# Performance work log

Hardware: AMD Instinct MI355X
Metric: run time of the kernel (lower is better)

Reference implementation:

```python
import jax, jax.numpy as jnp
import numpy as np


def setup_inputs() -> dict:
    key = jax.random.key(0)
    ks = jax.random.split(key, 4)
    B, T, D, H, C = 256, 512, 128, 512, 128
    # xavier-uniform-like scales
    def xavier(k, shape):
        fan_in, fan_out = shape
        lim = np.sqrt(6.0 / (fan_in + fan_out))
        return jax.random.uniform(k, shape, jnp.float32, -lim, lim)
    return {
        "x": jax.random.normal(ks[0], (B, T, D), jnp.float32),
        "Whx": xavier(ks[1], (D, H)),
        "Whh": xavier(ks[2], (H, H)),
        "Wph": xavier(ks[3], (H, C)),
        "bh": jnp.zeros((H,), jnp.float32),
        "bp": jnp.zeros((C,), jnp.float32),
    }


def reference(x, Whx, Whh, Wph, bh, bp):
    B, T, D = x.shape
    H = Whh.shape[0]
    # Precompute input projections for all timesteps in one big GEMM: [B,T,H]
    xproj = jnp.einsum("btd,dh->bth", x, Whx) + bh

    def step(h, xp_t):
        h = jnp.tanh(xp_t + h @ Whh)
        return h, None

    h0 = jnp.zeros((B, H), x.dtype)
    # scan over time: xproj transposed to [T,B,H]
    h_final, _ = jax.lax.scan(step, h0, jnp.swapaxes(xproj, 0, 1))
    return h_final @ Wph + bp
```

## Files before the change

### kernel.cpp

```cpp
#include <hip/hip_runtime.h>
#include <type_traits>

typedef _Float16 f16;
typedef f16 f16x4 __attribute__((ext_vector_type(4)));
typedef f16 f16x8 __attribute__((ext_vector_type(8)));
typedef float f32x4 __attribute__((ext_vector_type(4)));
typedef unsigned int u32;

#define MFMA __builtin_amdgcn_mfma_f32_16x16x32_f16

constexpr int Bsz = 256, T = 512, D = 128, H = 512, C = 128;
constexpr int ROWS = 16;
constexpr int TPB  = 512;
constexpr int LDH  = H + 8;
constexpr int LDX  = D + 8;
constexpr int NTG  = H / 16;
constexpr int PKT  = 8;
constexpr int KTL  = 3;
constexpr size_t XSTRIDE = (size_t)16 * NTG * 256;

__global__ void pack_w(const float* __restrict__ W, int K, int N, f16* __restrict__ out) {
    int total = K * N;
    int NT = N / 16;
    for (int idx = blockIdx.x * blockDim.x + threadIdx.x; idx < total;
         idx += gridDim.x * blockDim.x) {
        int e    = idx & 7;
        int lane = (idx >> 3) & 63;
        int tile = idx >> 9;
        int kt = tile / NT, nt = tile % NT;
        int k = kt * 32 + 8 * (lane >> 4) + e;
        int n = nt * 16 + (lane & 15);
        out[idx] = (f16)W[(size_t)k * N + n];
    }
}

__device__ __forceinline__ f16x8 load_a(const f16* base, int ld, int kt, int l15, int l4) {
    return *(const f16x8*)(base + l15 * ld + kt * 32 + 8 * l4);
}

__device__ __forceinline__ float fast_tanh(float v) {
    float e = __expf(2.f * v);
    return 1.f - __fdividef(2.f, e + 1.f);
}

template <typename OT>
__global__ __launch_bounds__(TPB, 2) void xproj_k(
    const float* __restrict__ x, const f16* __restrict__ wpack,
    const float* __restrict__ bh, OT* __restrict__ xp) {
    const f16* Whx_p = wpack;
    __shared__ __align__(16) f16 xb[2][ROWS][LDX];
    const int tid = threadIdx.x, lane = tid & 63, w = tid >> 6;
    const int l15 = lane & 15, l4 = lane >> 4;
    const int bt = blockIdx.x;
    const int t0 = blockIdx.y * 16;
    const int b0 = bt * ROWS;
    const int xrow = tid >> 5, xd0 = (tid & 31) * 4;
    const int ntg0 = w * 4;

    float bh4[4];
#pragma unroll
    for (int nt = 0; nt < 4; nt++) bh4[nt] = bh[(ntg0 + nt) * 16 + l15];
    {
        float4 v = *(const float4*)&x[((size_t)(b0 + xrow) * T + t0) * D + xd0];
        f16x4 h4 = {(f16)v.x, (f16)v.y, (f16)v.z, (f16)v.w};
        *(f16x4*)&xb[0][xrow][xd0] = h4;
    }
    __syncthreads();

    int p = 0;
    for (int tt = 0; tt < 16; tt++) {
        int t = t0 + tt;
        float4 xv;
        const bool havex = (tt + 1 < 16);
        if (havex)
            xv = *(const float4*)&x[((size_t)(b0 + xrow) * T + (t + 1)) * D + xd0];
        f32x4 acc[4];
#pragma unroll
        for (int nt = 0; nt < 4; nt++)
            acc[nt] = (f32x4){bh4[nt], bh4[nt], bh4[nt], bh4[nt]};
#pragma unroll
        for (int kt = 0; kt < D / 32; kt++) {
            f16x8 a = load_a(&xb[p][0][0], LDX, kt, l15, l4);
            const f16* btp = Whx_p + (((size_t)kt * NTG + ntg0) * 64 + lane) * 8;
#pragma unroll
            for (int nt = 0; nt < 4; nt++) {
                f16x8 b = *(const f16x8*)(btp + (size_t)nt * 512);
                acc[nt] = MFMA(a, b, acc[nt], 0, 0, 0);
            }
        }
        if (havex) {
            f16x4 h4 = {(f16)xv.x, (f16)xv.y, (f16)xv.z, (f16)xv.w};
            *(f16x4*)&xb[p ^ 1][xrow][xd0] = h4;
        }
        OT* op = xp + (((size_t)t * 16 + bt) * NTG + ntg0) * 256 + (size_t)lane * 4;
#pragma unroll
        for (int nt = 0; nt < 4; nt++) {
            if constexpr (std::is_same_v<OT, float>) {
                *(f32x4*)(op + (size_t)nt * 256) = acc[nt];
            } else {
                f16x4 v = {(f16)acc[nt][0], (f16)acc[nt][1], (f16)acc[nt][2],
                           (f16)acc[nt][3]};
                *(f16x4*)(op + (size_t)nt * 256) = v;
            }
        }
        __syncthreads();
        p ^= 1;
    }
}

template <int XP>
__global__ __launch_bounds__(TPB, 2) void rnn_main(
    const float* __restrict__ x, const f16* __restrict__ wpack,
    const void* __restrict__ xproj, const float* __restrict__ bh,
    const float* __restrict__ bp, float* __restrict__ out) {
    const f16* Whx_p = wpack;
    const f16* Whh_p = wpack + D * H;
    const f16* Wph_p = wpack + D * H + H * H;

    __shared__ __align__(16) f16 hbuf[2][ROWS][LDH];
    __shared__ __align__(16) f16 whh_lds[KTL * NTG * 64 * 8];
    __shared__ __align__(16) f16 xbuf[(XP == 0) ? 2 : 1][(XP == 0) ? ROWS : 1]
                                     [(XP == 0) ? LDX : 8];

    const int tid = threadIdx.x, lane = tid & 63, w = tid >> 6;
    const int l15 = lane & 15, l4 = lane >> 4;
    const int b0 = blockIdx.x * ROWS;
    const int xrow = tid >> 5, xd0 = (tid & 31) * 4;
    const int ntg0 = w * 4;

    f16x8 wreg[PKT][4];
#pragma unroll
    for (int kt = 0; kt < PKT; kt++)
#pragma unroll
        for (int nt = 0; nt < 4; nt++)
            wreg[kt][nt] =
                *(const f16x8*)(Whh_p + (((size_t)kt * NTG + ntg0 + nt) * 64 + lane) * 8);

    {
        const f16* src = Whh_p + (size_t)PKT * NTG * 512;
        for (int i = tid; i < KTL * NTG * 64; i += TPB)
            *(f16x8*)&whh_lds[(size_t)i * 8] = *(const f16x8*)(src + (size_t)i * 8);
    }
    for (int i = tid; i < ROWS * LDH; i += TPB) (&hbuf[0][0][0])[i] = (f16)0.f;

    float bh4[4];
    const float* xpf = nullptr;
    const f16* xph = nullptr;
    if constexpr (XP == 1) {
        xpf = (const float*)xproj + (((size_t)blockIdx.x * NTG + ntg0) * 64 + lane) * 4;
    } else if constexpr (XP == 2) {
        xph = (const f16*)xproj + (((size_t)blockIdx.x * NTG + ntg0) * 64 + lane) * 4;
    } else {
#pragma unroll
        for (int nt = 0; nt < 4; nt++) bh4[nt] = bh[(ntg0 + nt) * 16 + l15];
        float4 v = *(const float4*)&x[((size_t)(b0 + xrow) * T + 0) * D + xd0];
        f16x4 h4 = {(f16)v.x, (f16)v.y, (f16)v.z, (f16)v.w};
        *(f16x4*)&xbuf[0][xrow][xd0] = h4;
    }

    f16x8 sA[4], sB[4];
    {
        const f16* wb0 = Whh_p + ((size_t)ntg0 * 64 + lane) * 8;
#pragma unroll
        for (int nt = 0; nt < 4; nt++)
            sA[nt] = *(const f16x8*)(wb0 + ((size_t)11 * NTG + nt) * 512);
#pragma unroll
        for (int nt = 0; nt < 4; nt++)
            sB[nt] = *(const f16x8*)(wb0 + ((size_t)12 * NTG + nt) * 512);
    }
    __syncthreads();

    auto body = [&](int t, int pp, f16x8(&bA)[4], f16x8(&bB)[4]) {
        uintptr_t whu = (uintptr_t)Whh_p;
        asm volatile("" : "+s"(whu));
        const f16* wbase = (const f16*)whu + ((size_t)ntg0 * 64 + lane) * 8;
        u32 zo = 0;
        asm volatile("" : "+v"(zo));
        const f16x8* wlds = (const f16x8*)whh_lds + zo;

        f32x4 xr32[4];
        f16x4 xr16[4];
        if constexpr (XP == 1) {
            const float* xq = xpf + (size_t)t * XSTRIDE;
#pragma unroll
            for (int nt = 0; nt < 4; nt++) xr32[nt] = *(const f32x4*)(xq + (size_t)nt * 256);
        } else if constexpr (XP == 2) {
            const f16* xq = xph + (size_t)t * XSTRIDE;
#pragma unroll
            for (int nt = 0; nt < 4; nt++) xr16[nt] = *(const f16x4*)(xq + (size_t)nt * 256);
        }

        f32x4 acc[4];
        if constexpr (XP == 0) {
#pragma unroll
            for (int nt = 0; nt < 4; nt++)
                acc[nt] = (f32x4){bh4[nt], bh4[nt], bh4[nt], bh4[nt]};
        } else {
#pragma unroll
            for (int nt = 0; nt < 4; nt++) acc[nt] = (f32x4){0.f, 0.f, 0.f, 0.f};
        }

        const f16* hb = &hbuf[pp][0][0];

        if constexpr (XP == 0) {
            float4 xv;
            const bool havex = (t + 1 < T);
            if (havex)
                xv = *(const float4*)&x[((size_t)(b0 + xrow) * T + (t + 1)) * D + xd0];
            uintptr_t wxu = (uintptr_t)Whx_p;
            asm volatile("" : "+s"(wxu));
            const f16* wxs = (const f16*)wxu;
#pragma unroll
            for (int kt = 0; kt < D / 32; kt++) {
                f16x8 a = load_a(&xbuf[pp][0][0], LDX, kt, l15, l4);
                const f16* bt = wxs + (((size_t)kt * NTG + ntg0) * 64 + lane) * 8;
#pragma unroll
                for (int nt = 0; nt < 4; nt++) {
                    f16x8 b = *(const f16x8*)(bt + (size_t)nt * 512);
                    acc[nt] = MFMA(a, b, acc[nt], 0, 0, 0);
                }
            }
            if (havex) {
                f16x4 h4 = {(f16)xv.x, (f16)xv.y, (f16)xv.z, (f16)xv.w};
                *(f16x4*)&xbuf[pp ^ 1][xrow][xd0] = h4;
            }
        }

        auto LS = [&](int kt, f16x8(&bf)[4]) {
#pragma unroll
            for (int nt = 0; nt < 4; nt++)
                bf[nt] = *(const f16x8*)(wbase + ((size_t)kt * NTG + nt) * 512);
        };
        auto PK = [&](int kt) {
            f16x8 a = load_a(hb, LDH, kt, l15, l4);
#pragma unroll
            for (int nt = 0; nt < 4; nt++)
                acc[nt] = MFMA(a, wreg[kt][nt], acc[nt], 0, 0, 0);
        };
        auto CL = [&](int ktl) {
            f16x8 a = load_a(hb, LDH, PKT + ktl, l15, l4);
#pragma unroll
            for (int nt = 0; nt < 4; nt++)
                acc[nt] = MFMA(a, wlds[((size_t)ktl * NTG + ntg0 + nt) * 64 + lane],
                               acc[nt], 0, 0, 0);
        };
        auto CS = [&](int kt, f16x8(&bf)[4]) {
            f16x8 a = load_a(hb, LDH, kt, l15, l4);
#pragma unroll
            for (int nt = 0; nt < 4; nt++) acc[nt] = MFMA(a, bf[nt], acc[nt], 0, 0, 0);
        };

        PK(0); CS(11, bA); LS(13, bA);
        PK(1); CS(12, bB); LS(14, bB);
        PK(2); CL(0);
        PK(3); CL(1);
        PK(4); CL(2);
        PK(5); CS(13, bA); LS(15, bA);
        PK(6); CS(14, bB); LS(11, bB);
        PK(7); CS(15, bA); LS(12, bA);

#pragma unroll
        for (int nt = 0; nt < 4; nt++)
#pragma unroll
            for (int r = 0; r < 4; r++) {
                float v = acc[nt][r];
                if constexpr (XP == 1) v += xr32[nt][r];
                else if constexpr (XP == 2) v += (float)xr16[nt][r];
                float th = fast_tanh(v);
                hbuf[pp ^ 1][l4 * 4 + r][(ntg0 + nt) * 16 + l15] = (f16)th;
            }
        __syncthreads();
    };

    for (int t = 0; t < T; t += 2) {
        body(t, 0, sA, sB);
        body(t + 1, 1, sB, sA);
    }

    {
        float bpv = bp[w * 16 + l15];
        f32x4 acc = {bpv, bpv, bpv, bpv};
#pragma unroll 4
        for (int kt = 0; kt < H / 32; kt++) {
            f16x8 a = load_a(&hbuf[0][0][0], LDH, kt, l15, l4);
            f16x8 b = *(const f16x8*)(Wph_p + (((size_t)kt * (C / 16) + w) * 64 + lane) * 8);
            acc = MFMA(a, b, acc, 0, 0, 0);
        }
#pragma unroll
        for (int r = 0; r < 4; r++)
            out[(size_t)(b0 + l4 * 4 + r) * C + w * 16 + l15] = acc[r];
    }
}

extern "C" void kernel_launch(void* const* d_in, const int* in_sizes, int n_in,
                              void* d_out, int out_size, void* d_ws, size_t ws_size,
                              hipStream_t stream) {
    const float* x   = (const float*)d_in[0];
    const float* Whx = (const float*)d_in[1];
    const float* Whh = (const float*)d_in[2];
    const float* Wph = (const float*)d_in[3];
    const float* bh  = (const float*)d_in[4];
    const float* bp  = (const float*)d_in[5];

    f16* wp = (f16*)d_ws;
    pack_w<<<dim3(128), 256, 0, stream>>>(Whx, D, H, wp);
    pack_w<<<dim3(512), 256, 0, stream>>>(Whh, H, H, wp + D * H);
    pack_w<<<dim3(128), 256, 0, stream>>>(Wph, H, C, wp + D * H + H * H);

    const size_t wbytes = (size_t)(D * H + H * H + H * C) * sizeof(f16);
    const size_t xpel   = (size_t)T * 16 * NTG * 256;

    if (ws_size >= wbytes + xpel * sizeof(float)) {
        float* xpb = (float*)((char*)d_ws + wbytes);
        xproj_k<float><<<dim3(16, T / 16), TPB, 0, stream>>>(x, wp, bh, xpb);
        rnn_main<1><<<dim3(Bsz / ROWS), TPB, 0, stream>>>(x, wp, xpb, bh, bp,
                                                          (float*)d_out);
    } else if (ws_size >= wbytes + xpel * sizeof(f16)) {
        f16* xpb = (f16*)((char*)d_ws + wbytes);
        xproj_k<f16><<<dim3(16, T / 16), TPB, 0, stream>>>(x, wp, bh, xpb);
        rnn_main<2><<<dim3(Bsz / ROWS), TPB, 0, stream>>>(x, wp, xpb, bh, bp,
                                                          (float*)d_out);
    } else {
        rnn_main<0><<<dim3(Bsz / ROWS), TPB, 0, stream>>>(x, wp, nullptr, bh, bp,
                                                          (float*)d_out);
    }
}
```

Before: 1.652 ms.

## Replace per-step block barrier with per-wave LDS flags and triple-buffered hidden state

In the precomputed-projection variants, the per-timestep __syncthreads is replaced by per-wave progress flags in LDS. Each wave publishes its step counter with a release store, and consumers spin with acquire loads only before reading the K-slices produced by other waves. The hidden-state buffer becomes triple-buffered so a fast wave can write step t+1 while slower waves still read step t-1. The MFMA order is rearranged so each wave's remote dependencies are consumed as late as possible, at the cost of spin-wait overhead and a more fragile memory-ordering scheme.

```diff
diff --git a/kernel.cpp b/kernel.cpp
--- a/kernel.cpp
+++ b/kernel.cpp
@@ -117,8 +117,9 @@
     const f16* Whh_p = wpack + D * H;
     const f16* Wph_p = wpack + D * H + H * H;
 
-    __shared__ __align__(16) f16 hbuf[2][ROWS][LDH];
+    __shared__ __align__(16) f16 hbuf[3][ROWS][LDH];
     __shared__ __align__(16) f16 whh_lds[KTL * NTG * 64 * 8];
+    __shared__ u32 pflag[8];
     __shared__ __align__(16) f16 xbuf[(XP == 0) ? 2 : 1][(XP == 0) ? ROWS : 1]
                                      [(XP == 0) ? LDX : 8];
 
@@ -142,6 +143,7 @@
             *(f16x8*)&whh_lds[(size_t)i * 8] = *(const f16x8*)(src + (size_t)i * 8);
     }
     for (int i = tid; i < ROWS * LDH; i += TPB) (&hbuf[0][0][0])[i] = (f16)0.f;
+    if (tid < 8) pflag[tid] = 0u;
 
     float bh4[4];
     const float* xpf = nullptr;
@@ -170,7 +172,17 @@
     }
     __syncthreads();
 
-    auto body = [&](int t, int pp, f16x8(&bA)[4], f16x8(&bB)[4]) {
+    auto spin = [&](int v, u32 tgt) {
+        if constexpr (XP != 0) {
+            if (v != w)
+                while (__hip_atomic_load(&pflag[v], __ATOMIC_ACQUIRE,
+                                         __HIP_MEMORY_SCOPE_WORKGROUP) < tgt) {
+                }
+        }
+    };
+
+    auto body = [&](u32 t, const f16* hb, f16* hw, f16x8(&bA)[4], f16x8(&bB)[4],
+                    int pp) {
         uintptr_t whu = (uintptr_t)Whh_p;
         asm volatile("" : "+s"(whu));
         const f16* wbase = (const f16*)whu + ((size_t)ntg0 * 64 + lane) * 8;
@@ -199,8 +211,6 @@
 #pragma unroll
             for (int nt = 0; nt < 4; nt++) acc[nt] = (f32x4){0.f, 0.f, 0.f, 0.f};
         }
-
-        const f16* hb = &hbuf[pp][0][0];
 
         if constexpr (XP == 0) {
             float4 xv;
@@ -250,14 +260,17 @@
             for (int nt = 0; nt < 4; nt++) acc[nt] = MFMA(a, bf[nt], acc[nt], 0, 0, 0);
         };
 
-        PK(0); CS(11, bA); LS(13, bA);
-        PK(1); CS(12, bB); LS(14, bB);
-        PK(2); CL(0);
-        PK(3); CL(1);
-        PK(4); CL(2);
-        PK(5); CS(13, bA); LS(15, bA);
-        PK(6); CS(14, bB); LS(11, bB);
-        PK(7); CS(15, bA); LS(12, bA);
+        spin(0, t); PK(0); PK(1);
+        spin(5, t); CS(11, bA); LS(13, bA);
+        spin(1, t); PK(2); PK(3);
+        spin(6, t); CS(12, bB); LS(14, bB);
+        spin(2, t); PK(4); PK(5);
+                    CS(13, bA); LS(15, bA);
+        spin(3, t); PK(6); PK(7);
+                    CS(14, bB); LS(11, bB);
+        spin(4, t); CL(0); CL(1);
+                    CS(15, bA); LS(12, bA);
+                    CL(2);
 
 #pragma unroll
         for (int nt = 0; nt < 4; nt++)
@@ -267,22 +280,37 @@
                 if constexpr (XP == 1) v += xr32[nt][r];
                 else if constexpr (XP == 2) v += (float)xr16[nt][r];
                 float th = fast_tanh(v);
-                hbuf[pp ^ 1][l4 * 4 + r][(ntg0 + nt) * 16 + l15] = (f16)th;
-            }
-        __syncthreads();
+                hw[(l4 * 4 + r) * LDH + (ntg0 + nt) * 16 + l15] = (f16)th;
+            }
+        if constexpr (XP != 0) {
+            if (lane == 0)
+                __hip_atomic_store(&pflag[w], t + 1, __ATOMIC_RELEASE,
+                                   __HIP_MEMORY_SCOPE_WORKGROUP);
+        } else {
+            __syncthreads();
+        }
     };
 
-    for (int t = 0; t < T; t += 2) {
-        body(t, 0, sA, sB);
-        body(t + 1, 1, sB, sA);
-    }
-
+    f16* r0 = &hbuf[0][0][0];
+    f16* r1 = &hbuf[1][0][0];
+    f16* r2 = &hbuf[2][0][0];
+    for (u32 t = 0; t < T; t += 2) {
+        body(t,     r0, r1, sA, sB, 0);
+        body(t + 1, r1, r2, sB, sA, 1);
+        f16* n0 = r2; f16* n1 = r0; f16* n2 = r1;
+        r0 = n0; r1 = n1; r2 = n2;
+    }
+
+    if constexpr (XP != 0) {
+#pragma unroll
+        for (int v = 0; v < 8; v++) spin(v, (u32)T);
+    }
     {
         float bpv = bp[w * 16 + l15];
         f32x4 acc = {bpv, bpv, bpv, bpv};
 #pragma unroll 4
         for (int kt = 0; kt < H / 32; kt++) {
-            f16x8 a = load_a(&hbuf[0][0][0], LDH, kt, l15, l4);
+            f16x8 a = load_a(r0, LDH, kt, l15, l4);
             f16x8 b = *(const f16x8*)(Wph_p + (((size_t)kt * (C / 16) + w) * 64 + lane) * 8);
             acc = MFMA(a, b, acc, 0, 0, 0);
         }
```

Result: faster. 1.408 ms (-14.8%).

## Replace per-step block barrier with per-wave LDS flag handshake and ring buffer

Applied to the files above, without the earlier changes.

Each step's __syncthreads is replaced, on the precomputed-projection paths, by per-wave producer and consumer flags in LDS. Waves spin on these flags only for the K-chunks of h they need, and h lives in a 5-slot ring so fast waves can run up to four steps ahead. The K-chunk order is rotated per wave so each wave starts on its own freshly written chunk, and the weights moved out of LDS into streamed global loads shift from one chunk to two. The aim is to remove lock-step barrier stalls between waves, at the cost of spin-polling overhead, extra LDS for the ring, and more global weight traffic per step.

```diff
diff --git a/kernel.cpp b/kernel.cpp
--- a/kernel.cpp
+++ b/kernel.cpp
@@ -1,5 +1,6 @@
 #include <hip/hip_runtime.h>
 #include <type_traits>
+#include <utility>
 
 typedef _Float16 f16;
 typedef f16 f16x4 __attribute__((ext_vector_type(4)));
@@ -8,6 +9,7 @@
 typedef unsigned int u32;
 
 #define MFMA __builtin_amdgcn_mfma_f32_16x16x32_f16
+#define WGSCOPE __HIP_MEMORY_SCOPE_WORKGROUP
 
 constexpr int Bsz = 256, T = 512, D = 128, H = 512, C = 128;
 constexpr int ROWS = 16;
@@ -16,8 +18,40 @@
 constexpr int LDX  = D + 8;
 constexpr int NTG  = H / 16;
 constexpr int PKT  = 8;
-constexpr int KTL  = 3;
+constexpr int KTL  = 2;
+constexpr int NSTR = 6;
+constexpr int RING = 5;
+constexpr int SLOT = ROWS * LDH;
 constexpr size_t XSTRIDE = (size_t)16 * NTG * 256;
+
+struct Sched {
+    int kt[16];
+    int spin[16];
+    int sidx[16];
+    int skt[NSTR];
+};
+constexpr Sched make_sched(int V) {
+    Sched s{};
+    const int BASE[16] = {0, 10, 1, 11, 2, 3, 12, 4, 13, 5, 6, 14, 7, 15, 8, 9};
+    bool seen[8] = {};
+    seen[V] = true;
+    int si = 0;
+    for (int j = 0; j < 16; j++) {
+        int kt = (BASE[j] + 2 * V) & 15;
+        s.kt[j] = kt;
+        int u = kt >> 1;
+        s.spin[j] = seen[u] ? -1 : u;
+        seen[u] = true;
+        if (kt >= PKT + KTL) {
+            s.sidx[j] = si;
+            s.skt[si] = kt;
+            si++;
+        } else {
+            s.sidx[j] = -1;
+        }
+    }
+    return s;
+}
 
 __global__ void pack_w(const float* __restrict__ W, int K, int N, f16* __restrict__ out) {
     int total = K * N;
@@ -117,8 +151,10 @@
     const f16* Whh_p = wpack + D * H;
     const f16* Wph_p = wpack + D * H + H * H;
 
-    __shared__ __align__(16) f16 hbuf[2][ROWS][LDH];
+    __shared__ __align__(16) f16 hbuf[RING][ROWS][LDH];
     __shared__ __align__(16) f16 whh_lds[KTL * NTG * 64 * 8];
+    __shared__ int pflag[8];
+    __shared__ int cflag[8];
     __shared__ __align__(16) f16 xbuf[(XP == 0) ? 2 : 1][(XP == 0) ? ROWS : 1]
                                      [(XP == 0) ? LDX : 8];
 
@@ -126,7 +162,6 @@
     const int l15 = lane & 15, l4 = lane >> 4;
     const int b0 = blockIdx.x * ROWS;
     const int xrow = tid >> 5, xd0 = (tid & 31) * 4;
-    const int ntg0 = w * 4;
 
     f16x8 wreg[PKT][4];
 #pragma unroll
@@ -134,155 +169,223 @@
 #pragma unroll
         for (int nt = 0; nt < 4; nt++)
             wreg[kt][nt] =
-                *(const f16x8*)(Whh_p + (((size_t)kt * NTG + ntg0 + nt) * 64 + lane) * 8);
+                *(const f16x8*)(Whh_p + (((size_t)kt * NTG + w * 4 + nt) * 64 + lane) * 8);
 
     {
         const f16* src = Whh_p + (size_t)PKT * NTG * 512;
         for (int i = tid; i < KTL * NTG * 64; i += TPB)
             *(f16x8*)&whh_lds[(size_t)i * 8] = *(const f16x8*)(src + (size_t)i * 8);
     }
-    for (int i = tid; i < ROWS * LDH; i += TPB) (&hbuf[0][0][0])[i] = (f16)0.f;
+    for (int i = tid; i < SLOT; i += TPB) (&hbuf[0][0][0])[i] = (f16)0.f;
+    if (tid < 8) { pflag[tid] = 0; cflag[tid] = -1000; }
 
     float bh4[4];
     const float* xpf = nullptr;
     const f16* xph = nullptr;
     if constexpr (XP == 1) {
-        xpf = (const float*)xproj + (((size_t)blockIdx.x * NTG + ntg0) * 64 + lane) * 4;
+        xpf = (const float*)xproj + (((size_t)blockIdx.x * NTG + w * 4) * 64 + lane) * 4;
     } else if constexpr (XP == 2) {
-        xph = (const f16*)xproj + (((size_t)blockIdx.x * NTG + ntg0) * 64 + lane) * 4;
+        xph = (const f16*)xproj + (((size_t)blockIdx.x * NTG + w * 4) * 64 + lane) * 4;
     } else {
 #pragma unroll
-        for (int nt = 0; nt < 4; nt++) bh4[nt] = bh[(ntg0 + nt) * 16 + l15];
+        for (int nt = 0; nt < 4; nt++) bh4[nt] = bh[(w * 4 + nt) * 16 + l15];
         float4 v = *(const float4*)&x[((size_t)(b0 + xrow) * T + 0) * D + xd0];
         f16x4 h4 = {(f16)v.x, (f16)v.y, (f16)v.z, (f16)v.w};
         *(f16x4*)&xbuf[0][xrow][xd0] = h4;
     }
-
-    f16x8 sA[4], sB[4];
+    __syncthreads();
+
+    f16* const hbase = &hbuf[0][0][0];
+
+    auto run = [&](auto vc) {
+        constexpr int V = decltype(vc)::value;
+        constexpr Sched S = make_sched(V);
+        constexpr int ntg0 = V * 4;
+
+        auto pollp = [&](int tgt) -> u32 {
+            int f = __hip_atomic_load(&pflag[lane & 7], __ATOMIC_ACQUIRE, WGSCOPE);
+            return (u32)__ballot(f >= tgt) & 0xffu;
+        };
+        auto pollc = [&](int tgt) -> u32 {
+            int f = __hip_atomic_load(&cflag[lane & 7], __ATOMIC_ACQUIRE, WGSCOPE);
+            return (u32)__ballot(f >= tgt) & 0xffu;
+        };
+
+        f16x8 sb0[4], sb1[4];
+        {
+            const f16* wb0 = Whh_p + ((size_t)ntg0 * 64 + lane) * 8;
+#pragma unroll
+            for (int nt = 0; nt < 4; nt++)
+                sb0[nt] = *(const f16x8*)(wb0 + ((size_t)S.skt[0] * NTG + nt) * 512);
+#pragma unroll
+            for (int nt = 0; nt < 4; nt++)
+                sb1[nt] = *(const f16x8*)(wb0 + ((size_t)S.skt[1] * NTG + nt) * 512);
+        }
+
+        int sR = 0, sW = 1;
+#pragma unroll 1
+        for (int t = 0; t < T; t++) {
+            const f16* hb = hbase + sR * SLOT;
+            f16* hw = hbase + sW * SLOT;
+
+            uintptr_t whu = (uintptr_t)Whh_p;
+            asm volatile("" : "+s"(whu));
+            const f16* wbase = (const f16*)whu + ((size_t)ntg0 * 64 + lane) * 8;
+            u32 zo = 0;
+            asm volatile("" : "+v"(zo));
+            const f16x8* wlds = (const f16x8*)whh_lds + zo;
+
+            f32x4 xr32[4];
+            f16x4 xr16[4];
+            if constexpr (XP == 1) {
+                const float* xq = xpf + (size_t)t * XSTRIDE;
+#pragma unroll
+                for (int nt = 0; nt < 4; nt++)
+                    xr32[nt] = *(const f32x4*)(xq + (size_t)nt * 256);
+            } else if constexpr (XP == 2) {
+                const f16* xq = xph + (size_t)t * XSTRIDE;
+#pragma unroll
+                for (int nt = 0; nt < 4; nt++)
+                    xr16[nt] = *(const f16x4*)(xq + (size_t)nt * 256);
+            }
+
+            f32x4 acc[4];
+            if constexpr (XP == 0) {
+#pragma unroll
+                for (int nt = 0; nt < 4; nt++)
+                    acc[nt] = (f32x4){bh4[nt], bh4[nt], bh4[nt], bh4[nt]};
+            } else {
+#pragma unroll
+                for (int nt = 0; nt < 4; nt++) acc[nt] = (f32x4){0.f, 0.f, 0.f, 0.f};
+            }
+
+            if constexpr (XP == 0) {
+                float4 xv;
+                const bool havex = (t + 1 < T);
+                if (havex)
+                    xv = *(const float4*)&x[((size_t)(b0 + xrow) * T + (t + 1)) * D + xd0];
+                uintptr_t wxu = (uintptr_t)Whx_p;
+                asm volatile("" : "+s"(wxu));
+                const f16* wxs = (const f16*)wxu;
+#pragma unroll
+                for (int kt = 0; kt < D / 32; kt++) {
+                    f16x8 a = load_a(&xbuf[t & 1][0][0], LDX, kt, l15, l4);
+                    const f16* bt = wxs + (((size_t)kt * NTG + ntg0) * 64 + lane) * 8;
+#pragma unroll
+                    for (int nt = 0; nt < 4; nt++) {
+                        f16x8 b = *(const f16x8*)(bt + (size_t)nt * 512);
+                        acc[nt] = MFMA(a, b, acc[nt], 0, 0, 0);
+                    }
+                }
+                if (havex) {
+                    f16x4 h4 = {(f16)xv.x, (f16)xv.y, (f16)xv.z, (f16)xv.w};
+                    *(f16x4*)&xbuf[(t & 1) ^ 1][xrow][xd0] = h4;
+                }
+            }
+
+            u32 kmask = 1u << V;
+
+            auto pos = [&](auto jc) {
+                constexpr int j = decltype(jc)::value;
+                if constexpr (XP != 0 && S.spin[j] >= 0) {
+                    constexpr int u = S.spin[j];
+                    while (!((kmask >> u) & 1u)) kmask = pollp(t);
+                }
+                constexpr int kt = S.kt[j];
+                f16x8 a = load_a(hb, LDH, kt, l15, l4);
+                if constexpr (kt < PKT) {
+#pragma unroll
+                    for (int nt = 0; nt < 4; nt++)
+                        acc[nt] = MFMA(a, wreg[kt][nt], acc[nt], 0, 0, 0);
+                } else if constexpr (kt < PKT + KTL) {
+#pragma unroll
+                    for (int nt = 0; nt < 4; nt++)
+                        acc[nt] = MFMA(
+                            a, wlds[((size_t)(kt - PKT) * NTG + ntg0 + nt) * 64 + lane],
+                            acc[nt], 0, 0, 0);
+                } else {
+                    constexpr int i = S.sidx[j];
+                    constexpr int nk = S.skt[(i + 2) % NSTR];
+                    if constexpr ((i & 1) == 0) {
+#pragma unroll
+                        for (int nt = 0; nt < 4; nt++)
+                            acc[nt] = MFMA(a, sb0[nt], acc[nt], 0, 0, 0);
+#pragma unroll
+                        for (int nt = 0; nt < 4; nt++)
+                            sb0[nt] = *(const f16x8*)(wbase + ((size_t)nk * NTG + nt) * 512);
+                    } else {
+#pragma unroll
+                        for (int nt = 0; nt < 4; nt++)
+                            acc[nt] = MFMA(a, sb1[nt], acc[nt], 0, 0, 0);
+#pragma unroll
+                        for (int nt = 0; nt < 4; nt++)
+                            sb1[nt] = *(const f16x8*)(wbase + ((size_t)nk * NTG + nt) * 512);
+                    }
+                }
+            };
+#define POS(J) pos(std::integral_constant<int, J>{})
+            POS(0);  POS(1);  POS(2);  POS(3);
+            POS(4);  POS(5);  POS(6);  POS(7);
+            POS(8);  POS(9);  POS(10); POS(11);
+            POS(12); POS(13); POS(14); POS(15);
+#undef POS
+
+            if constexpr (XP != 0) {
+                if (lane == 0)
+                    __hip_atomic_store(&cflag[V], t, __ATOMIC_RELEASE, WGSCOPE);
+                int tgt = t - (RING - 1);
+                while (pollc(tgt) != 0xffu) {
+                }
+            }
+
+#pragma unroll
+            for (int nt = 0; nt < 4; nt++)
+#pragma unroll
+                for (int r = 0; r < 4; r++) {
+                    float v = acc[nt][r];
+                    if constexpr (XP == 1) v += xr32[nt][r];
+                    else if constexpr (XP == 2) v += (float)xr16[nt][r];
+                    float th = fast_tanh(v);
+                    hw[(l4 * 4 + r) * LDH + (ntg0 + nt) * 16 + l15] = (f16)th;
+                }
+            if constexpr (XP != 0) {
+                if (lane == 0)
+                    __hip_atomic_store(&pflag[V], t + 1, __ATOMIC_RELEASE, WGSCOPE);
+            } else {
+                __syncthreads();
+            }
+
+            sR = (sR + 1 == RING) ? 0 : sR + 1;
+            sW = (sW + 1 == RING) ? 0 : sW + 1;
+        }
+    };
+
+    switch (w) {
+        case 0: run(std::integral_constant<int, 0>{}); break;
+        case 1: run(std::integral_constant<int, 1>{}); break;
+        case 2: run(std::integral_constant<int, 2>{}); break;
+        case 3: run(std::integral_constant<int, 3>{}); break;
+        case 4: run(std::integral_constant<int, 4>{}); break;
+        case 5: run(std::integral_constant<int, 5>{}); break;
+        case 6: run(std::integral_constant<int, 6>{}); break;
+        default: run(std::integral_constant<int, 7>{}); break;
+    }
+
+    if constexpr (XP != 0) {
+        for (;;) {
+            int f = __hip_atomic_load(&pflag[lane & 7], __ATOMIC_ACQUIRE, WGSCOPE);
+            if (((u32)__ballot(f >= T) & 0xffu) == 0xffu) break;
+        }
+    } else {
+        __syncthreads();
+    }
     {
-        const f16* wb0 = Whh_p + ((size_t)ntg0 * 64 + lane) * 8;
-#pragma unroll
-        for (int nt = 0; nt < 4; nt++)
-            sA[nt] = *(const f16x8*)(wb0 + ((size_t)11 * NTG + nt) * 512);
-#pragma unroll
-        for (int nt = 0; nt < 4; nt++)
-            sB[nt] = *(const f16x8*)(wb0 + ((size_t)12 * NTG + nt) * 512);
-    }
-    __syncthreads();
-
-    auto body = [&](int t, int pp, f16x8(&bA)[4], f16x8(&bB)[4]) {
-        uintptr_t whu = (uintptr_t)Whh_p;
-        asm volatile("" : "+s"(whu));
-        const f16* wbase = (const f16*)whu + ((size_t)ntg0 * 64 + lane) * 8;
-        u32 zo = 0;
-        asm volatile("" : "+v"(zo));
-        const f16x8* wlds = (const f16x8*)whh_lds + zo;
-
-        f32x4 xr32[4];
-        f16x4 xr16[4];
-        if constexpr (XP == 1) {
-            const float* xq = xpf + (size_t)t * XSTRIDE;
-#pragma unroll
-            for (int nt = 0; nt < 4; nt++) xr32[nt] = *(const f32x4*)(xq + (size_t)nt * 256);
-        } else if constexpr (XP == 2) {
-            const f16* xq = xph + (size_t)t * XSTRIDE;
-#pragma unroll
-            for (int nt = 0; nt < 4; nt++) xr16[nt] = *(const f16x4*)(xq + (size_t)nt * 256);
-        }
-
-        f32x4 acc[4];
-        if constexpr (XP == 0) {
-#pragma unroll
-            for (int nt = 0; nt < 4; nt++)
-                acc[nt] = (f32x4){bh4[nt], bh4[nt], bh4[nt], bh4[nt]};
-        } else {
-#pragma unroll
-            for (int nt = 0; nt < 4; nt++) acc[nt] = (f32x4){0.f, 0.f, 0.f, 0.f};
-        }
-
-        const f16* hb = &hbuf[pp][0][0];
-
-        if constexpr (XP == 0) {
-            float4 xv;
-            const bool havex = (t + 1 < T);
-            if (havex)
-                xv = *(const float4*)&x[((size_t)(b0 + xrow) * T + (t + 1)) * D + xd0];
-            uintptr_t wxu = (uintptr_t)Whx_p;
-            asm volatile("" : "+s"(wxu));
-            const f16* wxs = (const f16*)wxu;
-#pragma unroll
-            for (int kt = 0; kt < D / 32; kt++) {
-                f16x8 a = load_a(&xbuf[pp][0][0], LDX, kt, l15, l4);
-                const f16* bt = wxs + (((size_t)kt * NTG + ntg0) * 64 + lane) * 8;
-#pragma unroll
-                for (int nt = 0; nt < 4; nt++) {
-                    f16x8 b = *(const f16x8*)(bt + (size_t)nt * 512);
-                    acc[nt] = MFMA(a, b, acc[nt], 0, 0, 0);
-                }
-            }
-            if (havex) {
-                f16x4 h4 = {(f16)xv.x, (f16)xv.y, (f16)xv.z, (f16)xv.w};
-                *(f16x4*)&xbuf[pp ^ 1][xrow][xd0] = h4;
-            }
-        }
-
-        auto LS = [&](int kt, f16x8(&bf)[4]) {
-#pragma unroll
-            for (int nt = 0; nt < 4; nt++)
-                bf[nt] = *(const f16x8*)(wbase + ((size_t)kt * NTG + nt) * 512);
-        };
-        auto PK = [&](int kt) {
-            f16x8 a = load_a(hb, LDH, kt, l15, l4);
-#pragma unroll
-            for (int nt = 0; nt < 4; nt++)
-                acc[nt] = MFMA(a, wreg[kt][nt], acc[nt], 0, 0, 0);
-        };
-        auto CL = [&](int ktl) {
-            f16x8 a = load_a(hb, LDH, PKT + ktl, l15, l4);
-#pragma unroll
-            for (int nt = 0; nt < 4; nt++)
-                acc[nt] = MFMA(a, wlds[((size_t)ktl * NTG + ntg0 + nt) * 64 + lane],
-                               acc[nt], 0, 0, 0);
-        };
-        auto CS = [&](int kt, f16x8(&bf)[4]) {
-            f16x8 a = load_a(hb, LDH, kt, l15, l4);
-#pragma unroll
-            for (int nt = 0; nt < 4; nt++) acc[nt] = MFMA(a, bf[nt], acc[nt], 0, 0, 0);
-        };
-
-        PK(0); CS(11, bA); LS(13, bA);
-        PK(1); CS(12, bB); LS(14, bB);
-        PK(2); CL(0);
-        PK(3); CL(1);
-        PK(4); CL(2);
-        PK(5); CS(13, bA); LS(15, bA);
-        PK(6); CS(14, bB); LS(11, bB);
-        PK(7); CS(15, bA); LS(12, bA);
-
-#pragma unroll
-        for (int nt = 0; nt < 4; nt++)
-#pragma unroll
-            for (int r = 0; r < 4; r++) {
-                float v = acc[nt][r];
-                if constexpr (XP == 1) v += xr32[nt][r];
-                else if constexpr (XP == 2) v += (float)xr16[nt][r];
-                float th = fast_tanh(v);
-                hbuf[pp ^ 1][l4 * 4 + r][(ntg0 + nt) * 16 + l15] = (f16)th;
-            }
-        __syncthreads();
-    };
-
-    for (int t = 0; t < T; t += 2) {
-        body(t, 0, sA, sB);
-        body(t + 1, 1, sB, sA);
-    }
-
-    {
+        const f16* hT = hbase + (T % RING) * SLOT;
         float bpv = bp[w * 16 + l15];
         f32x4 acc = {bpv, bpv, bpv, bpv};
 #pragma unroll 4
         for (int kt = 0; kt < H / 32; kt++) {
-            f16x8 a = load_a(&hbuf[0][0][0], LDH, kt, l15, l4);
+            f16x8 a = load_a(hT, LDH, kt, l15, l4);
             f16x8 b = *(const f16x8*)(Wph_p + (((size_t)kt * (C / 16) + w) * 64 + lane) * 8);
             acc = MFMA(a, b, acc, 0, 0, 0);
         }
```

New measurement: 1.449 ms. 1.14x faster.

## Process two batch tiles per block with flag-based wave sync and 3-slot h ring

Applied to the files above, without the earlier changes.

Each block now handles two 16-row batch tiles, using 8 blocks instead of 16, so every Whh B-fragment feeds two MFMAs. The per-step __syncthreads is replaced by per-wave LDS release/acquire flags, polled in a reordered K sequence, over a 3-deep hidden-state ring buffer so waves can run ahead. The LDS-resident Whh slices drop from 3 to 1 and the streamed ones rise to 7. The fp32 xproj path is removed in favour of the fp16 one. Using half as many CUs and adding spin-polling could lengthen the serial critical path.

```diff
diff --git a/kernel.cpp b/kernel.cpp
--- a/kernel.cpp
+++ b/kernel.cpp
@@ -1,5 +1,6 @@
 #include <hip/hip_runtime.h>
 #include <type_traits>
+#include <utility>
 
 typedef _Float16 f16;
 typedef f16 f16x4 __attribute__((ext_vector_type(4)));
@@ -8,16 +9,26 @@
 typedef unsigned int u32;
 
 #define MFMA __builtin_amdgcn_mfma_f32_16x16x32_f16
+#define WGSCOPE __HIP_MEMORY_SCOPE_WORKGROUP
 
 constexpr int Bsz = 256, T = 512, D = 128, H = 512, C = 128;
 constexpr int ROWS = 16;
 constexpr int TPB  = 512;
+constexpr int NBLK = 8;
+constexpr int NTPB = 2;
 constexpr int LDH  = H + 8;
 constexpr int LDX  = D + 8;
 constexpr int NTG  = H / 16;
 constexpr int PKT  = 8;
-constexpr int KTL  = 3;
+constexpr int KTL  = 1;
+constexpr int NSTR = 7;
+constexpr int RING = 3;
+constexpr int SLOT = ROWS * LDH;
 constexpr size_t XSTRIDE = (size_t)16 * NTG * 256;
+
+constexpr int KTO[16] = {0, 9, 1, 10, 2, 11, 3, 12, 4, 13, 5, 14, 6, 15, 7, 8};
+constexpr int SPN[16] = {0, 4, -1, 5, 1, -1, -1, 6, 2, -1, -1, 7, 3, -1, -1, -1};
+constexpr int SIX[16] = {-1, 0, -1, 1, -1, 2, -1, 3, -1, 4, -1, 5, -1, 6, -1, -1};
 
 __global__ void pack_w(const float* __restrict__ W, int K, int N, f16* __restrict__ out) {
     int total = K * N;
@@ -43,10 +54,9 @@
     return 1.f - __fdividef(2.f, e + 1.f);
 }
 
-template <typename OT>
 __global__ __launch_bounds__(TPB, 2) void xproj_k(
     const float* __restrict__ x, const f16* __restrict__ wpack,
-    const float* __restrict__ bh, OT* __restrict__ xp) {
+    const float* __restrict__ bh, f16* __restrict__ xp) {
     const f16* Whx_p = wpack;
     __shared__ __align__(16) f16 xb[2][ROWS][LDX];
     const int tid = threadIdx.x, lane = tid & 63, w = tid >> 6;
@@ -92,16 +102,12 @@
             f16x4 h4 = {(f16)xv.x, (f16)xv.y, (f16)xv.z, (f16)xv.w};
             *(f16x4*)&xb[p ^ 1][xrow][xd0] = h4;
         }
-        OT* op = xp + (((size_t)t * 16 + bt) * NTG + ntg0) * 256 + (size_t)lane * 4;
+        f16* op = xp + (((size_t)t * 16 + bt) * NTG + ntg0) * 256 + (size_t)lane * 4;
 #pragma unroll
         for (int nt = 0; nt < 4; nt++) {
-            if constexpr (std::is_same_v<OT, float>) {
-                *(f32x4*)(op + (size_t)nt * 256) = acc[nt];
-            } else {
-                f16x4 v = {(f16)acc[nt][0], (f16)acc[nt][1], (f16)acc[nt][2],
-                           (f16)acc[nt][3]};
-                *(f16x4*)(op + (size_t)nt * 256) = v;
-            }
+            f16x4 v = {(f16)acc[nt][0], (f16)acc[nt][1], (f16)acc[nt][2],
+                       (f16)acc[nt][3]};
+            *(f16x4*)(op + (size_t)nt * 256) = v;
         }
         __syncthreads();
         p ^= 1;
@@ -117,14 +123,16 @@
     const f16* Whh_p = wpack + D * H;
     const f16* Wph_p = wpack + D * H + H * H;
 
-    __shared__ __align__(16) f16 hbuf[2][ROWS][LDH];
+    __shared__ __align__(16) f16 hbuf[RING][NTPB][ROWS][LDH];
     __shared__ __align__(16) f16 whh_lds[KTL * NTG * 64 * 8];
-    __shared__ __align__(16) f16 xbuf[(XP == 0) ? 2 : 1][(XP == 0) ? ROWS : 1]
-                                     [(XP == 0) ? LDX : 8];
+    __shared__ int pflag[8];
+    __shared__ __align__(16) f16 xbuf[(XP == 0) ? 2 : 1][(XP == 0) ? NTPB : 1]
+                                     [(XP == 0) ? ROWS : 1][(XP == 0) ? LDX : 8];
 
     const int tid = threadIdx.x, lane = tid & 63, w = tid >> 6;
     const int l15 = lane & 15, l4 = lane >> 4;
-    const int b0 = blockIdx.x * ROWS;
+    const int bt0 = blockIdx.x, bt1 = blockIdx.x + NBLK;
+    const int b00 = bt0 * ROWS, b01 = bt1 * ROWS;
     const int xrow = tid >> 5, xd0 = (tid & 31) * 4;
     const int ntg0 = w * 4;
 
@@ -141,36 +149,52 @@
         for (int i = tid; i < KTL * NTG * 64; i += TPB)
             *(f16x8*)&whh_lds[(size_t)i * 8] = *(const f16x8*)(src + (size_t)i * 8);
     }
-    for (int i = tid; i < ROWS * LDH; i += TPB) (&hbuf[0][0][0])[i] = (f16)0.f;
+    for (int i = tid; i < NTPB * SLOT; i += TPB) (&hbuf[0][0][0][0])[i] = (f16)0.f;
+    if (tid < 8) pflag[tid] = 0;
 
     float bh4[4];
-    const float* xpf = nullptr;
-    const f16* xph = nullptr;
-    if constexpr (XP == 1) {
-        xpf = (const float*)xproj + (((size_t)blockIdx.x * NTG + ntg0) * 64 + lane) * 4;
-    } else if constexpr (XP == 2) {
-        xph = (const f16*)xproj + (((size_t)blockIdx.x * NTG + ntg0) * 64 + lane) * 4;
+    const f16* xph0 = nullptr;
+    const f16* xph1 = nullptr;
+    if constexpr (XP == 2) {
+        xph0 = (const f16*)xproj + (((size_t)bt0 * NTG + ntg0) * 64 + lane) * 4;
+        xph1 = (const f16*)xproj + (((size_t)bt1 * NTG + ntg0) * 64 + lane) * 4;
     } else {
 #pragma unroll
         for (int nt = 0; nt < 4; nt++) bh4[nt] = bh[(ntg0 + nt) * 16 + l15];
-        float4 v = *(const float4*)&x[((size_t)(b0 + xrow) * T + 0) * D + xd0];
-        f16x4 h4 = {(f16)v.x, (f16)v.y, (f16)v.z, (f16)v.w};
-        *(f16x4*)&xbuf[0][xrow][xd0] = h4;
-    }
-
-    f16x8 sA[4], sB[4];
+        float4 v0 = *(const float4*)&x[((size_t)(b00 + xrow) * T + 0) * D + xd0];
+        float4 v1 = *(const float4*)&x[((size_t)(b01 + xrow) * T + 0) * D + xd0];
+        f16x4 h0 = {(f16)v0.x, (f16)v0.y, (f16)v0.z, (f16)v0.w};
+        f16x4 h1 = {(f16)v1.x, (f16)v1.y, (f16)v1.z, (f16)v1.w};
+        *(f16x4*)&xbuf[0][0][xrow][xd0] = h0;
+        *(f16x4*)&xbuf[0][1][xrow][xd0] = h1;
+    }
+
+    f16x8 sb0[4], sb1[4];
     {
         const f16* wb0 = Whh_p + ((size_t)ntg0 * 64 + lane) * 8;
 #pragma unroll
         for (int nt = 0; nt < 4; nt++)
-            sA[nt] = *(const f16x8*)(wb0 + ((size_t)11 * NTG + nt) * 512);
+            sb0[nt] = *(const f16x8*)(wb0 + ((size_t)9 * NTG + nt) * 512);
 #pragma unroll
         for (int nt = 0; nt < 4; nt++)
-            sB[nt] = *(const f16x8*)(wb0 + ((size_t)12 * NTG + nt) * 512);
+            sb1[nt] = *(const f16x8*)(wb0 + ((size_t)10 * NTG + nt) * 512);
     }
     __syncthreads();
 
-    auto body = [&](int t, int pp, f16x8(&bA)[4], f16x8(&bB)[4]) {
+    f16* const hbase = &hbuf[0][0][0][0];
+
+    auto poll = [&](int tgt) -> u32 {
+        int f = __hip_atomic_load(&pflag[lane & 7], __ATOMIC_ACQUIRE, WGSCOPE);
+        return (u32)__ballot(f >= tgt) & 0xffu;
+    };
+
+    auto body = [&](int t, int sR, f16x8(&bA)[4], f16x8(&bB)[4]) {
+        const int sW = (sR + 1 == RING) ? 0 : sR + 1;
+        const f16* hb0 = hbase + sR * (NTPB * SLOT);
+        const f16* hb1 = hb0 + SLOT;
+        f16* hw0 = hbase + sW * (NTPB * SLOT);
+        f16* hw1 = hw0 + SLOT;
+
         uintptr_t whu = (uintptr_t)Whh_p;
         asm volatile("" : "+s"(whu));
         const f16* wbase = (const f16*)whu + ((size_t)ntg0 * 64 + lane) * 8;
@@ -178,117 +202,174 @@
         asm volatile("" : "+v"(zo));
         const f16x8* wlds = (const f16x8*)whh_lds + zo;
 
-        f32x4 xr32[4];
-        f16x4 xr16[4];
-        if constexpr (XP == 1) {
-            const float* xq = xpf + (size_t)t * XSTRIDE;
-#pragma unroll
-            for (int nt = 0; nt < 4; nt++) xr32[nt] = *(const f32x4*)(xq + (size_t)nt * 256);
-        } else if constexpr (XP == 2) {
-            const f16* xq = xph + (size_t)t * XSTRIDE;
-#pragma unroll
-            for (int nt = 0; nt < 4; nt++) xr16[nt] = *(const f16x4*)(xq + (size_t)nt * 256);
-        }
-
-        f32x4 acc[4];
+        f16x4 xr0[4], xr1[4];
+        if constexpr (XP == 2) {
+            const f16* xq0 = xph0 + (size_t)t * XSTRIDE;
+            const f16* xq1 = xph1 + (size_t)t * XSTRIDE;
+#pragma unroll
+            for (int nt = 0; nt < 4; nt++) {
+                xr0[nt] = *(const f16x4*)(xq0 + (size_t)nt * 256);
+                xr1[nt] = *(const f16x4*)(xq1 + (size_t)nt * 256);
+            }
+        }
+
+        f32x4 acc0[4], acc1[4];
         if constexpr (XP == 0) {
 #pragma unroll
-            for (int nt = 0; nt < 4; nt++)
-                acc[nt] = (f32x4){bh4[nt], bh4[nt], bh4[nt], bh4[nt]};
+            for (int nt = 0; nt < 4; nt++) {
+                acc0[nt] = (f32x4){bh4[nt], bh4[nt], bh4[nt], bh4[nt]};
+                acc1[nt] = acc0[nt];
+            }
         } else {
 #pragma unroll
-            for (int nt = 0; nt < 4; nt++) acc[nt] = (f32x4){0.f, 0.f, 0.f, 0.f};
-        }
-
-        const f16* hb = &hbuf[pp][0][0];
+            for (int nt = 0; nt < 4; nt++) {
+                acc0[nt] = (f32x4){0.f, 0.f, 0.f, 0.f};
+                acc1[nt] = (f32x4){0.f, 0.f, 0.f, 0.f};
+            }
+        }
 
         if constexpr (XP == 0) {
-            float4 xv;
+            float4 xv0, xv1;
             const bool havex = (t + 1 < T);
-            if (havex)
-                xv = *(const float4*)&x[((size_t)(b0 + xrow) * T + (t + 1)) * D + xd0];
+            if (havex) {
+                xv0 = *(const float4*)&x[((size_t)(b00 + xrow) * T + (t + 1)) * D + xd0];
+                xv1 = *(const float4*)&x[((size_t)(b01 + xrow) * T + (t + 1)) * D + xd0];
+            }
             uintptr_t wxu = (uintptr_t)Whx_p;
             asm volatile("" : "+s"(wxu));
             const f16* wxs = (const f16*)wxu;
 #pragma unroll
             for (int kt = 0; kt < D / 32; kt++) {
-                f16x8 a = load_a(&xbuf[pp][0][0], LDX, kt, l15, l4);
+                f16x8 a0 = load_a(&xbuf[t & 1][0][0][0], LDX, kt, l15, l4);
+                f16x8 a1 = load_a(&xbuf[t & 1][1][0][0], LDX, kt, l15, l4);
                 const f16* bt = wxs + (((size_t)kt * NTG + ntg0) * 64 + lane) * 8;
 #pragma unroll
                 for (int nt = 0; nt < 4; nt++) {
                     f16x8 b = *(const f16x8*)(bt + (size_t)nt * 512);
-                    acc[nt] = MFMA(a, b, acc[nt], 0, 0, 0);
+                    acc0[nt] = MFMA(a0, b, acc0[nt], 0, 0, 0);
+                    acc1[nt] = MFMA(a1, b, acc1[nt], 0, 0, 0);
                 }
             }
             if (havex) {
-                f16x4 h4 = {(f16)xv.x, (f16)xv.y, (f16)xv.z, (f16)xv.w};
-                *(f16x4*)&xbuf[pp ^ 1][xrow][xd0] = h4;
-            }
-        }
-
-        auto LS = [&](int kt, f16x8(&bf)[4]) {
-#pragma unroll
-            for (int nt = 0; nt < 4; nt++)
-                bf[nt] = *(const f16x8*)(wbase + ((size_t)kt * NTG + nt) * 512);
+                f16x4 h0 = {(f16)xv0.x, (f16)xv0.y, (f16)xv0.z, (f16)xv0.w};
+                f16x4 h1 = {(f16)xv1.x, (f16)xv1.y, (f16)xv1.z, (f16)xv1.w};
+                *(f16x4*)&xbuf[(t & 1) ^ 1][0][xrow][xd0] = h0;
+                *(f16x4*)&xbuf[(t & 1) ^ 1][1][xrow][xd0] = h1;
+            }
+        }
+
+        u32 kmask = 1u << w;
+
+        auto pos = [&](auto jc) {
+            constexpr int j = decltype(jc)::value;
+            if constexpr (XP != 0) {
+                constexpr int u = SPN[j];
+                if constexpr (u >= 0) {
+                    while (!((kmask >> u) & 1u)) kmask = poll(t);
+                }
+            }
+            constexpr int kt = KTO[j];
+            f16x8 a0 = load_a(hb0, LDH, kt, l15, l4);
+            f16x8 a1 = load_a(hb1, LDH, kt, l15, l4);
+            if constexpr (kt < PKT) {
+#pragma unroll
+                for (int nt = 0; nt < 4; nt++) {
+                    acc0[nt] = MFMA(a0, wreg[kt][nt], acc0[nt], 0, 0, 0);
+                    acc1[nt] = MFMA(a1, wreg[kt][nt], acc1[nt], 0, 0, 0);
+                }
+            } else if constexpr (kt < PKT + KTL) {
+#pragma unroll
+                for (int nt = 0; nt < 4; nt++) {
+                    f16x8 b = wlds[((size_t)(kt - PKT) * NTG + ntg0 + nt) * 64 + lane];
+                    acc0[nt] = MFMA(a0, b, acc0[nt], 0, 0, 0);
+                    acc1[nt] = MFMA(a1, b, acc1[nt], 0, 0, 0);
+                }
+            } else {
+                constexpr int i = SIX[j];
+                constexpr int nk = (i + 2 < NSTR) ? (9 + i + 2) : (9 + i + 2 - NSTR);
+                if constexpr ((i & 1) == 0) {
+#pragma unroll
+                    for (int nt = 0; nt < 4; nt++) {
+                        acc0[nt] = MFMA(a0, bA[nt], acc0[nt], 0, 0, 0);
+                        acc1[nt] = MFMA(a1, bA[nt], acc1[nt], 0, 0, 0);
+                    }
+#pragma unroll
+                    for (int nt = 0; nt < 4; nt++)
+                        bA[nt] = *(const f16x8*)(wbase + ((size_t)nk * NTG + nt) * 512);
+                } else {
+#pragma unroll
+                    for (int nt = 0; nt < 4; nt++) {
+                        acc0[nt] = MFMA(a0, bB[nt], acc0[nt], 0, 0, 0);
+                        acc1[nt] = MFMA(a1, bB[nt], acc1[nt], 0, 0, 0);
+                    }
+#pragma unroll
+                    for (int nt = 0; nt < 4; nt++)
+                        bB[nt] = *(const f16x8*)(wbase + ((size_t)nk * NTG + nt) * 512);
+                }
+            }
         };
-        auto PK = [&](int kt) {
-            f16x8 a = load_a(hb, LDH, kt, l15, l4);
-#pragma unroll
-            for (int nt = 0; nt < 4; nt++)
-                acc[nt] = MFMA(a, wreg[kt][nt], acc[nt], 0, 0, 0);
-        };
-        auto CL = [&](int ktl) {
-            f16x8 a = load_a(hb, LDH, PKT + ktl, l15, l4);
-#pragma unroll
-            for (int nt = 0; nt < 4; nt++)
-                acc[nt] = MFMA(a, wlds[((size_t)ktl * NTG + ntg0 + nt) * 64 + lane],
-                               acc[nt], 0, 0, 0);
-        };
-        auto CS = [&](int kt, f16x8(&bf)[4]) {
-            f16x8 a = load_a(hb, LDH, kt, l15, l4);
-#pragma unroll
-            for (int nt = 0; nt < 4; nt++) acc[nt] = MFMA(a, bf[nt], acc[nt], 0, 0, 0);
-        };
-
-        PK(0); CS(11, bA); LS(13, bA);
-        PK(1); CS(12, bB); LS(14, bB);
-        PK(2); CL(0);
-        PK(3); CL(1);
-        PK(4); CL(2);
-        PK(5); CS(13, bA); LS(15, bA);
-        PK(6); CS(14, bB); LS(11, bB);
-        PK(7); CS(15, bA); LS(12, bA);
+#define POS(J) pos(std::integral_constant<int, J>{})
+        POS(0);  POS(1);  POS(2);  POS(3);
+        POS(4);  POS(5);  POS(6);  POS(7);
+        POS(8);  POS(9);  POS(10); POS(11);
+        POS(12); POS(13); POS(14); POS(15);
+#undef POS
 
 #pragma unroll
         for (int nt = 0; nt < 4; nt++)
 #pragma unroll
             for (int r = 0; r < 4; r++) {
-                float v = acc[nt][r];
-                if constexpr (XP == 1) v += xr32[nt][r];
-                else if constexpr (XP == 2) v += (float)xr16[nt][r];
-                float th = fast_tanh(v);
-                hbuf[pp ^ 1][l4 * 4 + r][(ntg0 + nt) * 16 + l15] = (f16)th;
-            }
+                float v0 = acc0[nt][r];
+                float v1 = acc1[nt][r];
+                if constexpr (XP == 2) {
+                    v0 += (float)xr0[nt][r];
+                    v1 += (float)xr1[nt][r];
+                }
+                hw0[(l4 * 4 + r) * LDH + (ntg0 + nt) * 16 + l15] = (f16)fast_tanh(v0);
+                hw1[(l4 * 4 + r) * LDH + (ntg0 + nt) * 16 + l15] = (f16)fast_tanh(v1);
+            }
+        if constexpr (XP != 0) {
+            if (lane == 0)
+                __hip_atomic_store(&pflag[w], t + 1, __ATOMIC_RELEASE, WGSCOPE);
+        } else {
+            __syncthreads();
+        }
+    };
+
+    int sR = 0;
+#pragma unroll 1
+    for (int tt = 0; tt < T; tt += 2) {
+        body(tt, sR, sb0, sb1);
+        sR = (sR + 1 == RING) ? 0 : sR + 1;
+        body(tt + 1, sR, sb1, sb0);
+        sR = (sR + 1 == RING) ? 0 : sR + 1;
+    }
+
+    if constexpr (XP != 0) {
+        while (poll(T) != 0xffu) {
+        }
+    } else {
         __syncthreads();
-    };
-
-    for (int t = 0; t < T; t += 2) {
-        body(t, 0, sA, sB);
-        body(t + 1, 1, sB, sA);
-    }
-
+    }
     {
+        const f16* hT0 = hbase + (T % RING) * (NTPB * SLOT);
+        const f16* hT1 = hT0 + SLOT;
         float bpv = bp[w * 16 + l15];
-        f32x4 acc = {bpv, bpv, bpv, bpv};
+        f32x4 acc0 = {bpv, bpv, bpv, bpv};
+        f32x4 acc1 = acc0;
 #pragma unroll 4
         for (int kt = 0; kt < H / 32; kt++) {
-            f16x8 a = load_a(&hbuf[0][0][0], LDH, kt, l15, l4);
+            f16x8 a0 = load_a(hT0, LDH, kt, l15, l4);
+            f16x8 a1 = load_a(hT1, LDH, kt, l15, l4);
             f16x8 b = *(const f16x8*)(Wph_p + (((size_t)kt * (C / 16) + w) * 64 + lane) * 8);
-            acc = MFMA(a, b, acc, 0, 0, 0);
-        }
-#pragma unroll
-        for (int r = 0; r < 4; r++)
-            out[(size_t)(b0 + l4 * 4 + r) * C + w * 16 + l15] = acc[r];
+            acc0 = MFMA(a0, b, acc0, 0, 0, 0);
+            acc1 = MFMA(a1, b, acc1, 0, 0, 0);
+        }
+#pragma unroll
+        for (int r = 0; r < 4; r++) {
+            out[(size_t)(b00 + l4 * 4 + r) * C + w * 16 + l15] = acc0[r];
+            out[(size_t)(b01 + l4 * 4 + r) * C + w * 16 + l15] = acc1[r];
+        }
     }
 }
 
@@ -310,18 +391,13 @@
     const size_t wbytes = (size_t)(D * H + H * H + H * C) * sizeof(f16);
     const size_t xpel   = (size_t)T * 16 * NTG * 256;
 
-    if (ws_size >= wbytes + xpel * sizeof(float)) {
-        float* xpb = (float*)((char*)d_ws + wbytes);
-        xproj_k<float><<<dim3(16, T / 16), TPB, 0, stream>>>(x, wp, bh, xpb);
-        rnn_main<1><<<dim3(Bsz / ROWS), TPB, 0, stream>>>(x, wp, xpb, bh, bp,
-                                                          (float*)d_out);
-    } else if (ws_size >= wbytes + xpel * sizeof(f16)) {
+    if (ws_size >= wbytes + xpel * sizeof(f16)) {
         f16* xpb = (f16*)((char*)d_ws + wbytes);
-        xproj_k<f16><<<dim3(16, T / 16), TPB, 0, stream>>>(x, wp, bh, xpb);
-        rnn_main<2><<<dim3(Bsz / ROWS), TPB, 0, stream>>>(x, wp, xpb, bh, bp,
-                                                          (float*)d_out);
+        xproj_k<<<dim3(16, T / 16), TPB, 0, stream>>>(x, wp, bh, xpb);
+        rnn_main<2><<<dim3(NBLK), TPB, 0, stream>>>(x, wp, xpb, bh, bp,
+                                                    (float*)d_out);
     } else {
-        rnn_main<0><<<dim3(Bsz / ROWS), TPB, 0, stream>>>(x, wp, nullptr, bh, bp,
-                                                          (float*)d_out);
-    }
-}
+        rnn_main<0><<<dim3(NBLK), TPB, 0, stream>>>(x, wp, nullptr, bh, bp,
+                                                    (float*)d_out);
+    }
+}
```

After: 2.304 ms. 39.4% more time.
